# Kernel tuning notes

Hardware: AMD Instinct MI355X
Metric: run time of the kernel (lower is better)

## Reference

```python
import jax, jax.numpy as jnp
import numpy as np

KH, KW = 3, 3
STRIDE, PAD = 2, 1
NEG_SLOPE = 0.2
EPS = 1e-5


def conv2d(x, w, stride, pad):
    return jax.lax.conv_general_dilated(
        x, w, window_strides=(stride, stride),
        padding=[(pad, pad), (pad, pad)],
        dimension_numbers=('NCHW', 'OIHW', 'NCHW'))


def deform_conv2d(x, offsets, w_def):
    # x: [B,C,H,W]; offsets: [B,2*K,Ho,Wo] (per-kernel-tap (dy,dx) pairs);
    # w_def: [Cout,Cin,KH,KW]. Matches torchvision DeformConv2d (v1, no mask).
    B, C, H, W = x.shape
    Ho, Wo = offsets.shape[2], offsets.shape[3]
    K = KH * KW
    off = offsets.reshape(B, K, 2, Ho, Wo)
    dy, dx = off[:, :, 0], off[:, :, 1]            # [B,K,Ho,Wo]

    ky = jnp.arange(KH).repeat(KW).astype(x.dtype)   # [K]
    kx = jnp.tile(jnp.arange(KW), KH).astype(x.dtype)
    base_y = (jnp.arange(Ho) * STRIDE - PAD).astype(x.dtype)  # [Ho]
    base_x = (jnp.arange(Wo) * STRIDE - PAD).astype(x.dtype)

    # sampling positions [B,K,Ho,Wo]
    py = base_y[None, None, :, None] + ky[None, :, None, None] + dy
    px = base_x[None, None, None, :] + kx[None, :, None, None] + dx

    y0f = jnp.floor(py); x0f = jnp.floor(px)
    wy1 = py - y0f; wy0 = 1.0 - wy1
    wx1 = px - x0f; wx0 = 1.0 - wx1
    y0 = y0f.astype(jnp.int32); x0 = x0f.astype(jnp.int32)
    y1 = y0 + 1; x1 = x0 + 1

    xt = jnp.transpose(x, (0, 2, 3, 1))  # [B,H,W,C] for channel-last gather
    bidx = jnp.arange(B)[:, None, None, None]

    def corner(yi, xi):
        valid = ((yi >= 0) & (yi < H) & (xi >= 0) & (xi < W)).astype(x.dtype)
        yc = jnp.clip(yi, 0, H - 1); xc = jnp.clip(xi, 0, W - 1)
        v = xt[bidx, yc, xc]                         # [B,K,Ho,Wo,C]
        return v * valid[..., None]

    sampled = (corner(y0, x0) * (wy0 * wx0)[..., None]
               + corner(y0, x1) * (wy0 * wx1)[..., None]
               + corner(y1, x0) * (wy1 * wx0)[..., None]
               + corner(y1, x1) * (wy1 * wx1)[..., None])  # [B,K,Ho,Wo,C]

    wk = w_def.reshape(w_def.shape[0], w_def.shape[1], K)   # [Cout,Cin,K]
    return jnp.einsum('bkhwc,ock->bohw', sampled, wk)


def leaky_relu(x):
    return jnp.where(x >= 0, x, NEG_SLOPE * x)


def instance_norm(x):
    mean = jnp.mean(x, axis=(2, 3), keepdims=True)
    var = jnp.var(x, axis=(2, 3), keepdims=True)
    return (x - mean) * jax.lax.rsqrt(var + EPS)


def setup_inputs() -> dict:
    key = jax.random.key(0)
    k1, k2, k3, k4 = jax.random.split(key, 4)
    B, Cin, H, W = 8, 256, 128, 128
    Cout = 256
    x = jax.random.normal(k1, (B, Cin, H, W), dtype=jnp.float32)
    # conv_offset weight: predicts 2*K offset channels
    w_off = jax.random.normal(k2, (2 * KH * KW, Cin, KH, KW), dtype=jnp.float32) * 0.01
    w_def = jax.random.normal(k3, (Cout, Cin, KH, KW), dtype=jnp.float32) * 0.02
    w_1x1 = jax.random.normal(k4, (Cout, Cout, 1, 1), dtype=jnp.float32) * 0.02
    return {"x": x, "w_off": w_off, "w_def": w_def, "w_1x1": w_1x1}


def reference(x, w_off, w_def, w_1x1):
    offsets = conv2d(x, w_off, STRIDE, PAD)          # [B,18,Ho,Wo]
    y = deform_conv2d(x, offsets, w_def)             # [B,Cout,Ho,Wo]
    y = leaky_relu(y)
    y = conv2d(y, w_1x1, 1, 0)
    y = instance_norm(y)
    return leaky_relu(y)
```

## Files before the change

kernel.cpp:

```cpp
#include <hip/hip_runtime.h>

#define B_   8
#define CIN  256
#define H_   128
#define W_   128
#define HO   64
#define WO   64
#define CO_  256
#define NEG  0.2f

typedef __attribute__((ext_vector_type(8))) _Float16 h16x8;
typedef __attribute__((ext_vector_type(4))) float f32x4;
typedef unsigned short u16;

#define OFF_OFS   0
#define WDEF_OFS  589824
#define W1_OFS    884736
#define WBOFF_OFS 917504
#define Y1_OFS    954368
#define XBF_OFS   5148672

__device__ __forceinline__ float lrelu(float v) { return v >= 0.f ? v : NEG * v; }

__device__ __forceinline__ u16 f2h(float f) {
    _Float16 h = (_Float16)f;
    return *(u16*)&h;
}

__device__ __forceinline__ void gld16(const void* g, void* l) {
    __builtin_amdgcn_global_load_lds((const __attribute__((address_space(1))) unsigned*)g,
                                     (__attribute__((address_space(3))) unsigned*)l, 16, 0, 0);
}

__global__ __launch_bounds__(256) void prep(
    const float* __restrict__ wdef, const float* __restrict__ w1,
    const float* __restrict__ woff,
    u16* __restrict__ wdefh, u16* __restrict__ w1h, u16* __restrict__ wboff)
{
    int i = blockIdx.x * 256 + threadIdx.x;
    if (i < 9 * 256 * 256) {
        int c  = i & 255;
        int co = (i >> 8) & 255;
        int k  = i >> 16;
        wdefh[i] = f2h(wdef[((size_t)co * 256 + c) * 9 + k]);
    }
    if (i < 65536) w1h[i] = f2h(w1[i]);
    if (i < 73728) {
        int j  = i & 7;
        int s  = (i >> 3) & 7;
        int co = (i >> 6) & 31;
        int ch = (i >> 11) & 3;
        int k  = i >> 13;
        int c  = ch * 64 + ((s ^ ((co >> 1) & 7)) << 3) + j;
        wboff[i] = (co < 18) ? f2h(woff[((size_t)co * 256 + c) * 9 + k]) : (u16)0;
    }
}

__global__ __launch_bounds__(256) void nchw2nhwc(
    const float* __restrict__ x, u16* __restrict__ xh)
{
    __shared__ float tile[64][128];
    int bid = blockIdx.x;
    int g = bid & 3;
    int y = (bid >> 2) & 127;
    int b = bid >> 9;
    int t = threadIdx.x;

    const float* src = x + ((size_t)(b * 256 + g * 64) * 128 + y) * 128;
#pragma unroll
    for (int p = 0; p < 8; ++p) {
        int i = p * 256 + t;
        int cc = i >> 5, x4 = (i & 31) * 4;
        *(float4*)&tile[cc][x4] = *(const float4*)(src + (size_t)cc * 16384 + x4);
    }
    __syncthreads();

    int xpos = t >> 1, h = t & 1;
    u16 buf[32];
#pragma unroll
    for (int j = 0; j < 32; ++j) buf[j] = f2h(tile[h * 32 + j][xpos]);
    u16* dst = xh + (((size_t)b * 128 + y) * 128 + xpos) * 256 + g * 64 + h * 32;
#pragma unroll
    for (int q = 0; q < 4; ++q)
        *(int4*)(dst + q * 8) = *(int4*)(buf + q * 8);
}

__global__ __launch_bounds__(256) void offconv_mfma(
    const u16* __restrict__ xh, const u16* __restrict__ wboff,
    float* __restrict__ off)
{
    __shared__ __align__(16) char smem[57728];
    u16* xrowU = (u16*)smem;
    u16* bU    = (u16*)(smem + 49536);

    int blk = blockIdx.x;
    blk = (blk & 7) * 64 + (blk >> 3);
    int b = blk >> 6, ho = blk & 63;
    int t = threadIdx.x;
    int lane = t & 63, w = t >> 6;
    int r = lane & 15, kg = lane >> 4;

    const u16* xB = xh + (size_t)b * (128 * 128 * 256);

    f32x4 acc[2];
    acc[0] = f32x4{0.f, 0.f, 0.f, 0.f};
    acc[1] = f32x4{0.f, 0.f, 0.f, 0.f};

    if (t < 24) {
        int ry = t >> 3, s = t & 7;
        *(int4*)(smem + (ry * 129 * 8 + s) * 16) = int4{0, 0, 0, 0};
    }

    for (int ch = 0; ch < 4; ++ch) {
        __syncthreads();
        for (int ry = 0; ry < 3; ++ry) {
            int y = 2 * ho - 1 + ry;
            int rowbase = (ry * 129 + 1) * 128;
            if ((unsigned)y < 128u) {
#pragma unroll
                for (int p = 0; p < 4; ++p) {
                    int u = p * 256 + t;
                    int xpi = u >> 3, s = u & 7;
                    int c8 = s ^ (((xpi + 1) >> 1) & 7);
                    gld16(xB + ((size_t)(y * 128 + xpi)) * 256 + ch * 64 + c8 * 8,
                          smem + rowbase + p * 4096 + w * 1024);
                }
            } else if (ch == 0) {
#pragma unroll
                for (int p = 0; p < 4; ++p)
                    *(int4*)(smem + rowbase + (p * 256 + t) * 16) = int4{0, 0, 0, 0};
            }
        }
        gld16(wboff + (size_t)(0 * 4 + ch) * 2048 + t * 8,
              smem + 49536 + w * 1024);
        __syncthreads();

        for (int k = 0; k < 9; ++k) {
            int buf = k & 1;
            if (k < 8)
                gld16(wboff + (size_t)((k + 1) * 4 + ch) * 2048 + t * 8,
                      smem + 49536 + (buf ^ 1) * 4096 + w * 1024);
            int ky = k / 3, kx = k - 3 * ky;
            int pixA = w * 16 + r;
            int xp = 2 * pixA + kx;
            int abase = (ky * 129 + xp) * 64;
            int swA = (xp >> 1) & 7;
#pragma unroll
            for (int ksub = 0; ksub < 2; ++ksub) {
                int lc = ksub * 4 + kg;
                h16x8 a = *(h16x8*)(xrowU + abase + ((lc ^ swA) << 3));
#pragma unroll
                for (int n = 0; n < 2; ++n) {
                    int co = n * 16 + r;
                    h16x8 bb = *(h16x8*)(bU + buf * 2048 + co * 64 +
                                         ((lc ^ ((co >> 1) & 7)) << 3));
                    acc[n] = __builtin_amdgcn_mfma_f32_16x16x32_f16(a, bb, acc[n], 0, 0, 0);
                }
            }
            __syncthreads();
        }
    }

#pragma unroll
    for (int n = 0; n < 2; ++n) {
        int co = n * 16 + r;
        if (co < 18) {
#pragma unroll
            for (int j = 0; j < 4; ++j) {
                int wo = w * 16 + kg * 4 + j;
                off[(((size_t)b * 18 + co) * 64 + ho) * 64 + wo] = acc[n][j];
            }
        }
    }
}

__global__ __launch_bounds__(512, 4) void deform_nhwc(
    const u16* __restrict__ xh, const float* __restrict__ off,
    const u16* __restrict__ wdefh, u16* __restrict__ y1p)
{
    extern __shared__ __align__(16) char smem[];

    int blk = blockIdx.x;
    blk = (blk & 7) * 64 + (blk >> 3);
    int b = blk >> 6, ho = blk & 63;
    int t = threadIdx.x;
    int lane = t & 63, w = t >> 6;
    int r = lane & 15, kg = lane >> 4;
    int pixS = w * 8 + (lane >> 3);
    int cs   = lane & 7;

    f32x4 acc[4][2];
    f32x4 zz = {0.f, 0.f, 0.f, 0.f};
#pragma unroll
    for (int m = 0; m < 4; ++m)
#pragma unroll
        for (int n = 0; n < 2; ++n) acc[m][n] = zz;

    const u16* xB = xh + (size_t)b * (128 * 128 * 256);

    int o00, o01, o10, o11;
    float f00, f01, f10, f11;

    auto coords = [&](int k) {
        int ky = k / 3, kx = k - 3 * ky;
        float dy = off[(((size_t)b * 18 + 2 * k    ) * 64 + ho) * 64 + pixS];
        float dx = off[(((size_t)b * 18 + 2 * k + 1) * 64 + ho) * 64 + pixS];
        float py = (float)(ho * 2 - 1 + ky) + dy;
        float px = (float)(pixS * 2 - 1 + kx) + dx;
        float y0f = floorf(py), x0f = floorf(px);
        int y0 = (int)y0f, x0i = (int)x0f;
        float wy1 = py - y0f, wx1 = px - x0f;
        float wy0 = 1.f - wy1, wx0 = 1.f - wx1;
        int y1i = y0 + 1, x1i = x0i + 1;
        bool vy0 = (unsigned)y0  < 128u;
        bool vy1 = (unsigned)y1i < 128u;
        bool vx0 = (unsigned)x0i < 128u;
        bool vx1 = (unsigned)x1i < 128u;
        int yc0 = min(max(y0, 0), 127), yc1 = min(max(y1i, 0), 127);
        int xc0 = min(max(x0i, 0), 127), xc1 = min(max(x1i, 0), 127);
        o00 = yc0 * 128 + xc0;  o01 = yc0 * 128 + xc1;
        o10 = yc1 * 128 + xc0;  o11 = yc1 * 128 + xc1;
        f00 = (vy0 && vx0) ? wy0 * wx0 : 0.f;
        f01 = (vy0 && vx1) ? wy0 * wx1 : 0.f;
        f10 = (vy1 && vx0) ? wy1 * wx0 : 0.f;
        f11 = (vy1 && vx1) ? wy1 * wx1 : 0.f;
    };

    auto stage = [&](int k, int ch, int dbuf) {
        const u16* wk = wdefh + ((size_t)k << 16);
#pragma unroll
        for (int p2 = 0; p2 < 4; ++p2) {
            int i = p2 * 512 + t;
            int co = i >> 3, s = i & 7;
            gld16(wk + (size_t)co * 256 + ch * 64 + ((s ^ (co & 7)) << 3),
                  smem + dbuf * 32768 + p2 * 8192 + w * 1024);
        }
    };

    auto sample = [&](int ch, int dbuf) {
        int cw = ch * 64 + cs * 8;
        const u16* q00 = xB + (size_t)o00 * 256 + cw;
        const u16* q01 = xB + (size_t)o01 * 256 + cw;
        const u16* q10 = xB + (size_t)o10 * 256 + cw;
        const u16* q11 = xB + (size_t)o11 * 256 + cw;
        h16x8 c00 = *(const h16x8*)q00;
        h16x8 c01 = *(const h16x8*)q01;
        h16x8 c10 = *(const h16x8*)q10;
        h16x8 c11 = *(const h16x8*)q11;
        _Float16 hf00 = (_Float16)f00, hf01 = (_Float16)f01;
        _Float16 hf10 = (_Float16)f10, hf11 = (_Float16)f11;
        h16x8 v = c00 * hf00 + c01 * hf01 + c10 * hf10 + c11 * hf11;
        *(h16x8*)(smem + 65536 + dbuf * 8192 + pixS * 128 + ((cs ^ (pixS & 7)) << 4)) = v;
    };

    coords(0);
    stage(0, 0, 0);
    sample(0, 0);
    __syncthreads();

    for (int p = 0; p < 36; ++p) {
        int cur = p & 1;
        if (p < 35) {
            int pn = p + 1;
            int chn = pn / 9, kn = pn - 9 * chn;
            stage(kn, chn, cur ^ 1);
            coords(kn);
            sample(chn, cur ^ 1);
        }
        u16* wb = (u16*)(smem + cur * 32768);
        u16* sb = (u16*)(smem + 65536 + cur * 8192);
        h16x8 af[4], bfr[2];
        __builtin_amdgcn_s_setprio(1);
#pragma unroll
        for (int ksub = 0; ksub < 2; ++ksub) {
            int so = ((ksub * 4 + kg) ^ (r & 7)) << 3;
#pragma unroll
            for (int m = 0; m < 4; ++m)
                af[m] = *(h16x8*)(sb + (m * 16 + r) * 64 + so);
#pragma unroll
            for (int n = 0; n < 2; ++n)
                bfr[n] = *(h16x8*)(wb + (w * 32 + n * 16 + r) * 64 + so);
#pragma unroll
            for (int m = 0; m < 4; ++m)
#pragma unroll
                for (int n = 0; n < 2; ++n)
                    acc[m][n] = __builtin_amdgcn_mfma_f32_16x16x32_f16(af[m], bfr[n], acc[m][n], 0, 0, 0);
        }
        __builtin_amdgcn_s_setprio(0);
        __syncthreads();
    }

    u16* outT = (u16*)smem;
    int rg = lane >> 4;
#pragma unroll
    for (int m = 0; m < 4; ++m)
#pragma unroll
        for (int n = 0; n < 2; ++n) {
            int co = w * 32 + n * 16 + r;
#pragma unroll
            for (int j = 0; j < 4; ++j) {
                int prow = m * 16 + rg * 4 + j;
                outT[prow * 256 + co] = f2h(lrelu(acc[m][n][j]));
            }
        }
    __syncthreads();
    u16* dst = y1p + (size_t)(b * 64 + ho) * 16384;
#pragma unroll
    for (int p = 0; p < 4; ++p)
        *(int4*)((char*)dst + p * 8192 + t * 16) = *(int4*)(smem + p * 8192 + t * 16);
}

__global__ __launch_bounds__(256) void conv1x1_mfma(
    const u16* __restrict__ y1p, const u16* __restrict__ w1h,
    float* __restrict__ out)
{
    __shared__ __align__(16) char smem[20480];
    u16* btile = (u16*)smem;
    u16* atile = (u16*)(smem + 16384);

    int blk = blockIdx.x;
    blk = (blk & 7) * 64 + (blk >> 3);
    int b = blk >> 6, ho = blk & 63;
    int t = threadIdx.x, lane = t & 63, w = t >> 6;
    int r = lane & 15, kg = lane >> 4;
    int sR = (r >> 1) & 3;

    f32x4 acc[4][4];
    f32x4 zz = {0.f, 0.f, 0.f, 0.f};
#pragma unroll
    for (int m = 0; m < 4; ++m)
#pragma unroll
        for (int n = 0; n < 4; ++n) acc[m][n] = zz;

    const u16* abase = y1p + (size_t)(b * 64 + ho) * 16384;

    for (int ch = 0; ch < 8; ++ch) {
#pragma unroll
        for (int p = 0; p < 4; ++p) {
            int slot = p * 256 + t;
            int o = slot >> 2, qq = slot & 3;
            gld16(w1h + o * 256 + ch * 32 + ((qq ^ ((o >> 1) & 3)) << 3),
                  smem + p * 4096 + (t >> 6) * 1024);
        }
        {
            int pix = t >> 2, qq = t & 3;
            gld16(abase + pix * 256 + ch * 32 + ((qq ^ ((pix >> 1) & 3)) << 3),
                  smem + 16384 + (t >> 6) * 1024);
        }
        __syncthreads();
        h16x8 af[4], bfr[4];
#pragma unroll
        for (int m = 0; m < 4; ++m)
            af[m] = *(h16x8*)(atile + (m * 16 + r) * 32 + ((kg ^ sR) << 3));
#pragma unroll
        for (int n = 0; n < 4; ++n)
            bfr[n] = *(h16x8*)(btile + (w * 64 + n * 16 + r) * 32 + ((kg ^ sR) << 3));
#pragma unroll
        for (int m = 0; m < 4; ++m)
#pragma unroll
            for (int n = 0; n < 4; ++n)
                acc[m][n] = __builtin_amdgcn_mfma_f32_16x16x32_f16(af[m], bfr[n], acc[m][n], 0, 0, 0);
        __syncthreads();
    }

    int rg = lane >> 4;
#pragma unroll
    for (int m = 0; m < 4; ++m)
#pragma unroll
        for (int n = 0; n < 4; ++n) {
            int o = w * 64 + n * 16 + r;
            int pix0 = m * 16 + rg * 4;
            float4 v;
            v.x = acc[m][n][0]; v.y = acc[m][n][1];
            v.z = acc[m][n][2]; v.w = acc[m][n][3];
            *(float4*)(out + ((size_t)(b * 256 + o) * 64 + ho) * 64 + pix0) = v;
        }
}

__global__ __launch_bounds__(256) void instnorm(float* __restrict__ out)
{
    int bc = blockIdx.x;
    float* p = out + (size_t)bc * 4096;
    int t = threadIdx.x;

    float4 v[4];
    float s1 = 0.f, s2 = 0.f;
#pragma unroll
    for (int i = 0; i < 4; ++i) {
        v[i] = *(const float4*)&p[(t + i * 256) * 4];
        s1 += v[i].x + v[i].y + v[i].z + v[i].w;
        s2 += v[i].x * v[i].x + v[i].y * v[i].y + v[i].z * v[i].z + v[i].w * v[i].w;
    }
#pragma unroll
    for (int o = 32; o > 0; o >>= 1) {
        s1 += __shfl_down(s1, o);
        s2 += __shfl_down(s2, o);
    }
    __shared__ float rs[8];
    __shared__ float mb[2];
    int wave = t >> 6;
    if ((t & 63) == 0) { rs[wave] = s1; rs[4 + wave] = s2; }
    __syncthreads();
    if (t == 0) {
        float a = rs[0] + rs[1] + rs[2] + rs[3];
        float qq = rs[4] + rs[5] + rs[6] + rs[7];
        float mean = a * (1.f / 4096.f);
        float var  = qq * (1.f / 4096.f) - mean * mean;
        mb[0] = mean;
        mb[1] = rsqrtf(var + 1e-5f);
    }
    __syncthreads();
    float mean = mb[0], inv = mb[1];
#pragma unroll
    for (int i = 0; i < 4; ++i) {
        float4 u = v[i];
        u.x = lrelu((u.x - mean) * inv);
        u.y = lrelu((u.y - mean) * inv);
        u.z = lrelu((u.z - mean) * inv);
        u.w = lrelu((u.w - mean) * inv);
        *(float4*)&p[(t + i * 256) * 4] = u;
    }
}

extern "C" void kernel_launch(void* const* d_in, const int* in_sizes, int n_in,
                              void* d_out, int out_size, void* d_ws, size_t ws_size,
                              hipStream_t stream)
{
    const float* x     = (const float*)d_in[0];
    const float* w_off = (const float*)d_in[1];
    const float* w_def = (const float*)d_in[2];
    const float* w1    = (const float*)d_in[3];
    float* out = (float*)d_out;
    float* ws  = (float*)d_ws;

    float* off   = ws + OFF_OFS;
    u16*   wdefh = (u16*)(ws + WDEF_OFS);
    u16*   w1h   = (u16*)(ws + W1_OFS);
    u16*   wboff = (u16*)(ws + WBOFF_OFS);
    u16*   y1p   = (u16*)(ws + Y1_OFS);
    u16*   xh    = (u16*)(ws + XBF_OFS);

    hipFuncSetAttribute((const void*)deform_nhwc,
                        hipFuncAttributeMaxDynamicSharedMemorySize, 81920);

    hipLaunchKernelGGL(prep,         dim3(2304), dim3(256), 0, stream, w_def, w1, w_off, wdefh, w1h, wboff);
    hipLaunchKernelGGL(nchw2nhwc,    dim3(4096), dim3(256), 0, stream, x, xh);
    hipLaunchKernelGGL(offconv_mfma, dim3(512),  dim3(256), 0, stream, xh, wboff, off);
    hipLaunchKernelGGL(deform_nhwc,  dim3(512),  dim3(512), 81920, stream, xh, off, wdefh, y1p);
    hipLaunchKernelGGL(conv1x1_mfma, dim3(512),  dim3(256), 0, stream, y1p, w1h, out);
    hipLaunchKernelGGL(instnorm,     dim3(2048), dim3(256), 0, stream, out);
}
```

Baseline: 156.4 us.

## Precompute bilinear tap descriptors in separate kernel for deformable conv

Adds a tapgen kernel that turns each pixel/tap offset into a packed int4 descriptor (corner base address, dx/dy step bits, four masked fp16 bilinear weights). The deformable conv kernel then reads that descriptor in place of redoing floor, clamp, validity and weight maths for every channel chunk. This moves the per-chunk index math out of the hot loop, at the cost of an extra launch, a workspace buffer of about 4.7 MB, and fp16 rounding of the interpolation weights. The path is only taken when the workspace is large enough; otherwise the old inline kernel runs.

```diff
diff --git a/kernel.cpp b/kernel.cpp
--- a/kernel.cpp
+++ b/kernel.cpp
@@ -19,6 +19,8 @@
 #define WBOFF_OFS 917504
 #define Y1_OFS    954368
 #define XBF_OFS   5148672
+#define TAP_OFS   21925888
+#define WS_NEED_TAP ((21925888ull + 1179648ull) * 4ull)
 
 __device__ __forceinline__ float lrelu(float v) { return v >= 0.f ? v : NEG * v; }
 
@@ -174,7 +176,155 @@
     }
 }
 
-__global__ __launch_bounds__(512, 4) void deform_nhwc(
+__global__ __launch_bounds__(256) void tapgen(
+    const float* __restrict__ off, int4* __restrict__ tap)
+{
+    int bid = blockIdx.x;
+    int b = bid >> 6, ho = bid & 63;
+    for (int i = threadIdx.x; i < 576; i += 256) {
+        int pix = i / 9, k = i - 9 * (i / 9);
+        int ky = k / 3, kx = k - 3 * ky;
+        float dy = off[(((size_t)b * 18 + 2 * k    ) * 64 + ho) * 64 + pix];
+        float dx = off[(((size_t)b * 18 + 2 * k + 1) * 64 + ho) * 64 + pix];
+        float py = (float)(ho * 2 - 1 + ky) + dy;
+        float px = (float)(pix * 2 - 1 + kx) + dx;
+        float y0f = floorf(py), x0f = floorf(px);
+        int y0 = (int)y0f, x0i = (int)x0f;
+        float wy1 = py - y0f, wx1 = px - x0f;
+        float wy0 = 1.f - wy1, wx0 = 1.f - wx1;
+        int y1i = y0 + 1, x1i = x0i + 1;
+        bool vy0 = (unsigned)y0  < 128u;
+        bool vy1 = (unsigned)y1i < 128u;
+        bool vx0 = (unsigned)x0i < 128u;
+        bool vx1 = (unsigned)x1i < 128u;
+        int yc0 = min(max(y0, 0), 127), yc1 = min(max(y1i, 0), 127);
+        int xc0 = min(max(x0i, 0), 127), xc1 = min(max(x1i, 0), 127);
+        int4 e;
+        e.x = (yc0 * 128 + xc0) * 512 | (xc1 - xc0) | ((yc1 - yc0) << 1);
+        e.y = (int)((unsigned)f2h((vy0 && vx0) ? wy0 * wx0 : 0.f) |
+                    ((unsigned)f2h((vy0 && vx1) ? wy0 * wx1 : 0.f) << 16));
+        e.z = (int)((unsigned)f2h((vy1 && vx0) ? wy1 * wx0 : 0.f) |
+                    ((unsigned)f2h((vy1 && vx1) ? wy1 * wx1 : 0.f) << 16));
+        e.w = 0;
+        tap[(size_t)bid * 576 + i] = e;
+    }
+}
+
+__global__ __launch_bounds__(512, 4) void deform_tap(
+    const u16* __restrict__ xh, const int4* __restrict__ tap,
+    const u16* __restrict__ wdefh, u16* __restrict__ y1p)
+{
+    extern __shared__ __align__(16) char smem[];
+
+    int blk = blockIdx.x;
+    blk = (blk & 7) * 64 + (blk >> 3);
+    int b = blk >> 6, ho = blk & 63;
+    int t = threadIdx.x;
+    int lane = t & 63, w = t >> 6;
+    int r = lane & 15, kg = lane >> 4;
+    int pixS = w * 8 + (lane >> 3);
+    int cs   = lane & 7;
+
+    f32x4 acc[4][2];
+    f32x4 zz = {0.f, 0.f, 0.f, 0.f};
+#pragma unroll
+    for (int m = 0; m < 4; ++m)
+#pragma unroll
+        for (int n = 0; n < 2; ++n) acc[m][n] = zz;
+
+    const int4* tapB = tap + (size_t)(b * 64 + ho) * 576 + pixS * 9;
+    const char* xb2  = (const char*)(xh + (size_t)b * (128 * 128 * 256)) + cs * 16;
+
+    int sbw = pixS * 128 + ((cs ^ (pixS & 7)) << 4);
+
+    auto stage = [&](int k, int ch, int dbuf) {
+        const u16* wk = wdefh + ((size_t)k << 16);
+#pragma unroll
+        for (int p2 = 0; p2 < 4; ++p2) {
+            int i = p2 * 512 + t;
+            int co = i >> 3, s = i & 7;
+            gld16(wk + (size_t)co * 256 + ch * 64 + ((s ^ (co & 7)) << 3),
+                  smem + dbuf * 32768 + p2 * 8192 + w * 1024);
+        }
+    };
+
+    auto sample = [&](int k, int ch, int dbuf) {
+        int4 e = tapB[k];
+        int o00 = e.x & 0x7FFFFE00;
+        int dx  = (e.x & 1) << 9;
+        int dy  = (e.x & 2) << 15;
+        const char* base = xb2 + ch * 128;
+        h16x8 c00 = *(const h16x8*)(base + o00);
+        h16x8 c01 = *(const h16x8*)(base + o00 + dx);
+        h16x8 c10 = *(const h16x8*)(base + o00 + dy);
+        h16x8 c11 = *(const h16x8*)(base + o00 + dy + dx);
+        union U { int u; _Float16 h[2]; };
+        U u01, u23;
+        u01.u = e.y; u23.u = e.z;
+        h16x8 v = c00 * u01.h[0] + c01 * u01.h[1] + c10 * u23.h[0] + c11 * u23.h[1];
+        *(h16x8*)(smem + 65536 + dbuf * 8192 + sbw) = v;
+    };
+
+    auto mfmaPhase = [&](int cur) {
+        u16* wb = (u16*)(smem + cur * 32768);
+        u16* sb = (u16*)(smem + 65536 + cur * 8192);
+        h16x8 af[4], bfr[2];
+        __builtin_amdgcn_s_setprio(1);
+#pragma unroll
+        for (int ksub = 0; ksub < 2; ++ksub) {
+            int so = ((ksub * 4 + kg) ^ (r & 7)) << 3;
+#pragma unroll
+            for (int m = 0; m < 4; ++m)
+                af[m] = *(h16x8*)(sb + (m * 16 + r) * 64 + so);
+#pragma unroll
+            for (int n = 0; n < 2; ++n)
+                bfr[n] = *(h16x8*)(wb + (w * 32 + n * 16 + r) * 64 + so);
+#pragma unroll
+            for (int m = 0; m < 4; ++m)
+#pragma unroll
+                for (int n = 0; n < 2; ++n)
+                    acc[m][n] = __builtin_amdgcn_mfma_f32_16x16x32_f16(af[m], bfr[n], acc[m][n], 0, 0, 0);
+        }
+        __builtin_amdgcn_s_setprio(0);
+        __syncthreads();
+    };
+
+    stage(0, 0, 0);
+    sample(0, 0, 0);
+    __syncthreads();
+
+    for (int p = 0; p < 36; ++p) {
+        int cur = p & 1;
+        if (p < 35) {
+            int pn = p + 1;
+            int chn = pn / 9, kn = pn - 9 * chn;
+            stage(kn, chn, cur ^ 1);
+            sample(kn, chn, cur ^ 1);
+        }
+        mfmaPhase(cur);
+    }
+
+    u16* outT = (u16*)smem;
+    int rg = lane >> 4;
+#pragma unroll
+    for (int m = 0; m < 4; ++m)
+#pragma unroll
+        for (int n = 0; n < 2; ++n) {
+            int co = w * 32 + n * 16 + r;
+#pragma unroll
+            for (int j = 0; j < 4; ++j) {
+                int prow = m * 16 + rg * 4 + j;
+                outT[prow * 256 + co] = f2h(lrelu(acc[m][n][j]));
+            }
+        }
+    __syncthreads();
+    u16* dst = y1p + (size_t)(b * 64 + ho) * 16384;
+#pragma unroll
+    for (int p = 0; p < 4; ++p)
+        *(int4*)((char*)dst + p * 8192 + t * 16) = *(int4*)(smem + p * 8192 + t * 16);
+}
+
+__global__ __launch_bounds__(512, 4) void deform_inline(
     const u16* __restrict__ xh, const float* __restrict__ off,
     const u16* __restrict__ wdefh, u16* __restrict__ y1p)
 {
@@ -439,14 +589,24 @@
     u16*   wboff = (u16*)(ws + WBOFF_OFS);
     u16*   y1p   = (u16*)(ws + Y1_OFS);
     u16*   xh    = (u16*)(ws + XBF_OFS);
-
-    hipFuncSetAttribute((const void*)deform_nhwc,
+    int4*  tap   = (int4*)(ws + TAP_OFS);
+
+    const bool use_tap = ws_size >= WS_NEED_TAP;
+
+    hipFuncSetAttribute((const void*)deform_tap,
+                        hipFuncAttributeMaxDynamicSharedMemorySize, 81920);
+    hipFuncSetAttribute((const void*)deform_inline,
                         hipFuncAttributeMaxDynamicSharedMemorySize, 81920);
 
     hipLaunchKernelGGL(prep,         dim3(2304), dim3(256), 0, stream, w_def, w1, w_off, wdefh, w1h, wboff);
     hipLaunchKernelGGL(nchw2nhwc,    dim3(4096), dim3(256), 0, stream, x, xh);
     hipLaunchKernelGGL(offconv_mfma, dim3(512),  dim3(256), 0, stream, xh, wboff, off);
-    hipLaunchKernelGGL(deform_nhwc,  dim3(512),  dim3(512), 81920, stream, xh, off, wdefh, y1p);
+    if (use_tap) {
+        hipLaunchKernelGGL(tapgen,     dim3(512), dim3(256), 0, stream, off, tap);
+        hipLaunchKernelGGL(deform_tap, dim3(512), dim3(512), 81920, stream, xh, tap, wdefh, y1p);
+    } else {
+        hipLaunchKernelGGL(deform_inline, dim3(512), dim3(512), 81920, stream, xh, off, wdefh, y1p);
+    }
     hipLaunchKernelGGL(conv1x1_mfma, dim3(512),  dim3(256), 0, stream, y1p, w1h, out);
     hipLaunchKernelGGL(instnorm,     dim3(2048), dim3(256), 0, stream, out);
 }
```

Result: no change. 155.5 us (-0.6%).
